# Kernel tuning notes

Hardware: AMD Instinct MI355X
Metric: run time of the kernel (lower is better)

The kernel has to match this reference:

```python
import jax, jax.numpy as jnp
import numpy as np

EMBED = 50
SEQ = 100
NLABEL = 15
HID = 20
VOCAB = 50000
BATCH = 8192


def gru_scan(xs, W, U, b, return_sequences):
    """Keras GRUCell (reset_after=True, gate order z,r,h).
    xs: (B, T, D). W: (D, 3H), U: (H, 3H), b: (2, 3H) [input bias, recurrent bias].
    """
    B = xs.shape[0]
    H = U.shape[0]
    bi, br = b[0], b[1]
    h0 = jnp.zeros((B, H), dtype=xs.dtype)

    def step(h, x_t):
        mx = x_t @ W + bi                      # (B, 3H)
        mh = h @ U + br                        # (B, 3H)
        xz, xr, xh = mx[:, :H], mx[:, H:2*H], mx[:, 2*H:]
        hz, hr, hh_ = mh[:, :H], mh[:, H:2*H], mh[:, 2*H:]
        z = jax.nn.sigmoid(xz + hz)
        r = jax.nn.sigmoid(xr + hr)
        hh = jnp.tanh(xh + r * hh_)
        h_new = z * h + (1.0 - z) * hh
        return h_new, h_new

    xs_t = jnp.swapaxes(xs, 0, 1)              # (T, B, D)
    h_last, hs = jax.lax.scan(step, h0, xs_t)
    if return_sequences:
        return jnp.swapaxes(hs, 0, 1)          # (B, T, H)
    return h_last                               # (B, H)


def setup_inputs() -> dict:
    key = jax.random.key(0)
    ks = jax.random.split(key, 9)
    s = 0.05
    return {
        "x": jax.random.randint(ks[0], (BATCH, SEQ), 0, VOCAB),
        "emb_table": jax.random.normal(ks[1], (VOCAB, EMBED), jnp.float32) * s,
        "W1": jax.random.normal(ks[2], (EMBED, 3 * HID), jnp.float32) * s,
        "U1": jax.random.normal(ks[3], (HID, 3 * HID), jnp.float32) * s,
        "b1": jnp.zeros((2, 3 * HID), jnp.float32),
        "W2": jax.random.normal(ks[4], (HID, 3 * HID), jnp.float32) * s,
        "U2": jax.random.normal(ks[5], (HID, 3 * HID), jnp.float32) * s,
        "b2": jnp.zeros((2, 3 * HID), jnp.float32),
        "Wd": jax.random.normal(ks[6], (HID, NLABEL), jnp.float32) * s,
        "bd": jnp.zeros((NLABEL,), jnp.float32),
        "drop_rate": 0,
    }


def reference(x, emb_table, W1, U1, b1, W2, U2, b2, Wd, bd, drop_rate):
    emb = emb_table[x]                               # (B, T, E)
    seq = gru_scan(emb, W1, U1, b1, return_sequences=True)   # (B, T, H)
    enc = gru_scan(seq, W2, U2, b2, return_sequences=False)  # (B, H)
    # drop_rate == 0 -> tf.nn.dropout is identity
    logits = enc @ Wd + bd                           # (B, 15)
    return logits
```

## Files before the change

### kernel.cpp

```cpp
#include <hip/hip_runtime.h>
#include <hip/hip_bf16.h>
#include <hip/hip_fp16.h>

#define SEQ_T 100
#define HID 20
#define EMB_D 50
#define VOCAB_N 50000
#define TABW 60
#define NTILE 3125
#define BBLK 782

typedef short sh8 __attribute__((ext_vector_type(8)));
typedef float f4  __attribute__((ext_vector_type(4)));

#define OFF_U1P 0
#define OFF_W2P 600
#define OFF_U2P 1200
#define OFF_B1  3600
#define OFF_B2  3720
#define OFF_WD  3840
#define OFF_BD  4140
#define OFF_TAB 4160

__device__ __forceinline__ float ldf(const void* p, int i, int isf) {
  return isf ? ((const float*)p)[i]
             : __bfloat162float(((const __hip_bfloat16*)p)[i]);
}
__device__ __forceinline__ short f2bf(float f) {
  unsigned u = __float_as_uint(f);
  u += 0x7fffu + ((u >> 16) & 1u);
  return (short)(u >> 16);
}
__device__ __forceinline__ float rdl(float v, int l) {
  return __uint_as_float(__builtin_amdgcn_readlane(__float_as_uint(v), l));
}
__device__ __forceinline__ int detect_isf(const void* emb) {
  uint4 dv = ((const uint4*)emb)[threadIdx.x & 63];
  int big = 0;
#pragma unroll
  for (int i = 0; i < 4; ++i) {
    unsigned w = ((const unsigned*)&dv)[i];
    big |= (((w >> 7) & 0xFF) >= 140) | (((w >> 23) & 0xFF) >= 140);
  }
  return (__ballot(big) != 0ull) ? 1 : 0;
}

__global__ __launch_bounds__(256) void build_table(
    const void* __restrict__ emb, const void* __restrict__ W1,
    const void* __restrict__ b1,
    const void* __restrict__ U1, const void* __restrict__ W2,
    const void* __restrict__ U2, const void* __restrict__ b2,
    const void* __restrict__ Wd, const void* __restrict__ bd,
    float* __restrict__ ws)
{
  const int isf = detect_isf(emb);
  if (blockIdx.x == 0) {
    const int t = threadIdx.x;
    unsigned* wsu = (unsigned*)ws;
    for (int i = t; i < 600; i += 256) {
      const int j = i / 10, p = i % 10;
      const int k0 = 2 * p, k1 = 2 * p + 1;
#define PK(M) ((unsigned)__half_as_ushort(__float2half_rn(ldf(M, k0 * 60 + j, isf))) | \
               ((unsigned)__half_as_ushort(__float2half_rn(ldf(M, k1 * 60 + j, isf))) << 16))
      wsu[OFF_U1P + i] = PK(U1);
      wsu[OFF_W2P + i] = PK(W2);
      wsu[OFF_U2P + i] = PK(U2);
#undef PK
    }
    for (int i = t; i < 120; i += 256) {
      ws[OFF_B1 + i] = ldf(b1, i, isf);
      ws[OFF_B2 + i] = ldf(b2, i, isf);
    }
    for (int i = t; i < 300; i += 256) ws[OFF_WD + i] = ldf(Wd, i, isf);
    for (int i = t; i < 15;  i += 256) ws[OFF_BD + i] = ldf(bd, i, isf);
  }

  const int L = threadIdx.x & 63, q = L >> 4, c = L & 15;
  const int wid = blockIdx.x * 4 + (threadIdx.x >> 6);
  float* __restrict__ tab = ws + OFF_TAB;

  __shared__ int4 sB[64][8];
  if (threadIdx.x < 64) {
#pragma unroll
    for (int nt = 0; nt < 4; ++nt) {
      const int col = nt * 16 + c;
      sh8 B0, B1;
#pragma unroll
      for (int jj = 0; jj < 8; ++jj) {
        const int k0 = q * 8 + jj, k1 = 32 + q * 8 + jj;
        B0[jj] = (col < TABW) ? f2bf(ldf(W1, k0 * TABW + col, isf)) : (short)0;
        B1[jj] = (col < TABW && k1 < EMB_D)
                     ? f2bf(ldf(W1, k1 * TABW + col, isf)) : (short)0;
      }
      sB[L][nt * 2]     = *(const int4*)&B0;
      sB[L][nt * 2 + 1] = *(const int4*)&B1;
    }
  }
  float bi[4];
#pragma unroll
  for (int nt = 0; nt < 4; ++nt) {
    const int col = nt * 16 + c;
    bi[nt] = (col < TABW) ? ldf(b1, col, isf) : 0.f;
  }
  __syncthreads();

  for (int tile = wid; tile < NTILE; tile += BBLK * 4) {
    const int v0 = tile * 16;
    sh8 A0, A1;
#pragma unroll
    for (int jj = 0; jj < 8; ++jj) { A0[jj] = 0; A1[jj] = 0; }
    if (!isf) {
      const unsigned short* eb = (const unsigned short*)emb;
      const size_t rb = (size_t)(v0 + c) * EMB_D;
#pragma unroll
      for (int i = 0; i < 4; ++i) {
        unsigned d = *(const unsigned*)(eb + rb + q * 8 + 2 * i);
        A0[2 * i] = (short)(d & 0xffff); A0[2 * i + 1] = (short)(d >> 16);
      }
      const int k1b = 32 + q * 8;
#pragma unroll
      for (int i = 0; i < 4; ++i) {
        const int k = k1b + 2 * i;
        if (k + 1 < EMB_D) {
          unsigned d = *(const unsigned*)(eb + rb + k);
          A1[2 * i] = (short)(d & 0xffff); A1[2 * i + 1] = (short)(d >> 16);
        }
      }
    } else {
      const float* ef = (const float*)emb;
      const size_t rb = (size_t)(v0 + c) * EMB_D;
#pragma unroll
      for (int jj = 0; jj < 8; ++jj) {
        const int k0 = q * 8 + jj, k1 = 32 + q * 8 + jj;
        A0[jj] = f2bf(ef[rb + k0]);
        A1[jj] = (k1 < EMB_D) ? f2bf(ef[rb + k1]) : (short)0;
      }
    }
#pragma unroll
    for (int nt = 0; nt < 4; ++nt) {
      int4 b0i = sB[L][nt * 2], b1i = sB[L][nt * 2 + 1];
      sh8 B0 = *(const sh8*)&b0i, B1 = *(const sh8*)&b1i;
      const int col = nt * 16 + c;
      f4 acc = { bi[nt], bi[nt], bi[nt], bi[nt] };
      acc = __builtin_amdgcn_mfma_f32_16x16x32_bf16(A0, B0, acc, 0, 0, 0);
      acc = __builtin_amdgcn_mfma_f32_16x16x32_bf16(A1, B1, acc, 0, 0, 0);
      if (col < TABW) {
#pragma unroll
        for (int r = 0; r < 4; ++r)
          tab[(size_t)(v0 + q * 4 + r) * TABW + col] = acc[r];
      }
    }
  }
}

__global__ __launch_bounds__(256, 8) void gru_main(
    const int* __restrict__ x, const float* __restrict__ ws,
    const void* __restrict__ emb, void* __restrict__ out)
{
  const int isf = detect_isf(emb);
  const int j = threadIdx.x & 63;
  const int e = __builtin_amdgcn_readfirstlane(blockIdx.x * 4 + (threadIdx.x >> 6));
  const int jc = j < TABW ? j : 0;

  const int* xr = x + (size_t)e * SEQ_T;
  const float* tab = ws + OFF_TAB;
  const int o1 = jc * 40;
  const int jc4 = jc * 4;
  const int a1 = ((j - 20) & 63) * 4;
  const int a2 = ((j + 40) & 63) * 4;
  const float br1 = ws[OFF_B1 + 60 + jc];
  const float bi2 = ws[OFF_B2 + jc];
  const float br2 = ws[OFF_B2 + 60 + jc];
  float h2out;

  asm volatile(
    "global_load_dwordx4 v[10:13], %[o1], %[wsp] offset:0\n\t"
    "global_load_dwordx4 v[14:17], %[o1], %[wsp] offset:16\n\t"
    "global_load_dwordx2 v[18:19], %[o1], %[wsp] offset:32\n\t"
    "v_add_u32 v44, 0x960, %[o1]\n\t"
    "v_add_u32 v45, 0x12c0, %[o1]\n\t"
    "global_load_dwordx4 v[20:23], v44, %[wsp] offset:0\n\t"
    "global_load_dwordx4 v[24:27], v44, %[wsp] offset:16\n\t"
    "global_load_dwordx2 v[28:29], v44, %[wsp] offset:32\n\t"
    "global_load_dwordx4 v[30:33], v45, %[wsp] offset:0\n\t"
    "global_load_dwordx4 v[34:37], v45, %[wsp] offset:16\n\t"
    "global_load_dwordx2 v[38:39], v45, %[wsp] offset:32\n\t"
    "s_mov_b64 s[20:21], 0\n\ts_mov_b64 s[22:23], 0\n\t"
    "s_mov_b64 s[24:25], 0\n\ts_mov_b64 s[26:27], 0\n\t"
    "s_mov_b64 s[28:29], 0\n\t"
    "s_mov_b64 s[30:31], 0\n\ts_mov_b64 s[32:33], 0\n\t"
    "s_mov_b64 s[34:35], 0\n\ts_mov_b64 s[36:37], 0\n\t"
    "s_mov_b64 s[38:39], 0\n\t"
    "v_mov_b32 v40, 0\n\t"
    "v_mov_b32 v41, 0\n\t"
    "s_load_dword s65, %[xp], 0x0\n\t"
    "s_load_dword s66, %[xp], 0x4\n\t"
    "s_waitcnt lgkmcnt(0)\n\t"
    "s_mul_i32 s65, s65, 240\n\t"
    "s_mul_i32 s66, s66, 240\n\t"
    "v_add_u32 v50, s65, %[jc4]\n\t"
    "global_load_dword v42, v50, %[tabp]\n\t"
    "v_add_u32 v50, s66, %[jc4]\n\t"
    "global_load_dword v43, v50, %[tabp]\n\t"
    "s_load_dword s65, %[xp], 0x8\n\t"
    "s_movk_i32 s64, 0xc\n\t"
    "s_movk_i32 s67, 0x64\n\t"
    "s_waitcnt vmcnt(0)\n\t"
    "0:\n\t"
    "v_mov_b32 v44, %[br1]\n\t"
    "v_dot2_f32_f16 v44, s20, v10, v44\n\t"
    "v_dot2_f32_f16 v44, s21, v11, v44\n\t"
    "v_dot2_f32_f16 v44, s22, v12, v44\n\t"
    "v_dot2_f32_f16 v44, s23, v13, v44\n\t"
    "v_dot2_f32_f16 v44, s24, v14, v44\n\t"
    "v_dot2_f32_f16 v44, s25, v15, v44\n\t"
    "v_dot2_f32_f16 v44, s26, v16, v44\n\t"
    "v_dot2_f32_f16 v44, s27, v17, v44\n\t"
    "v_dot2_f32_f16 v44, s28, v18, v44\n\t"
    "v_dot2_f32_f16 v44, s29, v19, v44\n\t"
    "v_add_f32 v45, v42, v44\n\t"
    "v_mul_f32 v45, 0xbfb8aa3b, v45\n\t"
    "v_exp_f32 v45, v45\n\t"
    "s_nop 1\n\t"
    "v_add_f32 v45, 1.0, v45\n\t"
    "v_rcp_f32 v45, v45\n\t"
    "s_nop 1\n\t"
    "ds_bpermute_b32 v46, %[a1], v45\n\t"
    "s_waitcnt lgkmcnt(0)\n\t"
    "v_fma_f32 v47, v46, v44, v42\n\t"
    "v_mul_f32 v47, 0x4038aa3b, v47\n\t"
    "v_exp_f32 v47, v47\n\t"
    "s_nop 1\n\t"
    "v_add_f32 v47, 1.0, v47\n\t"
    "v_rcp_f32 v47, v47\n\t"
    "s_nop 1\n\t"
    "v_fma_f32 v47, -2.0, v47, 1.0\n\t"
    "ds_bpermute_b32 v46, %[a2], v47\n\t"
    "s_waitcnt lgkmcnt(0)\n\t"
    "v_sub_f32 v48, v40, v46\n\t"
    "v_fma_f32 v40, v45, v48, v46\n\t"
    "s_nop 1\n\t"
    "v_cvt_f16_f32 v46, v40\n\t"
    "s_nop 1\n\t"
    "ds_swizzle_b32 v47, v46 offset:0x041F\n\t"
    "s_waitcnt lgkmcnt(0)\n\t"
    "v_pack_b32_f16 v46, v46, v47\n\t"
    "s_nop 1\n\t"
    "v_readlane_b32 s20, v46, 0\n\t"
    "v_readlane_b32 s21, v46, 2\n\t"
    "v_readlane_b32 s22, v46, 4\n\t"
    "v_readlane_b32 s23, v46, 6\n\t"
    "v_readlane_b32 s24, v46, 8\n\t"
    "v_readlane_b32 s25, v46, 10\n\t"
    "v_readlane_b32 s26, v46, 12\n\t"
    "v_readlane_b32 s27, v46, 14\n\t"
    "v_readlane_b32 s28, v46, 16\n\t"
    "v_readlane_b32 s29, v46, 18\n\t"
    "s_mul_i32 s66, s65, 240\n\t"
    "v_add_u32 v50, s66, %[jc4]\n\t"
    "s_waitcnt vmcnt(0)\n\t"
    "v_mov_b32 v42, v43\n\t"
    "global_load_dword v43, v50, %[tabp]\n\t"
    "s_min_u32 s64, s64, 396\n\t"
    "s_load_dword s65, %[xp], s64\n\t"
    "s_add_u32 s64, s64, 4\n\t"
    "v_mov_b32 v44, %[bi2]\n\t"
    "v_mov_b32 v48, %[br2]\n\t"
    "v_dot2_f32_f16 v44, s20, v20, v44\n\t"
    "v_dot2_f32_f16 v48, s30, v30, v48\n\t"
    "v_dot2_f32_f16 v44, s21, v21, v44\n\t"
    "v_dot2_f32_f16 v48, s31, v31, v48\n\t"
    "v_dot2_f32_f16 v44, s22, v22, v44\n\t"
    "v_dot2_f32_f16 v48, s32, v32, v48\n\t"
    "v_dot2_f32_f16 v44, s23, v23, v44\n\t"
    "v_dot2_f32_f16 v48, s33, v33, v48\n\t"
    "v_dot2_f32_f16 v44, s24, v24, v44\n\t"
    "v_dot2_f32_f16 v48, s34, v34, v48\n\t"
    "v_dot2_f32_f16 v44, s25, v25, v44\n\t"
    "v_dot2_f32_f16 v48, s35, v35, v48\n\t"
    "v_dot2_f32_f16 v44, s26, v26, v44\n\t"
    "v_dot2_f32_f16 v48, s36, v36, v48\n\t"
    "v_dot2_f32_f16 v44, s27, v27, v44\n\t"
    "v_dot2_f32_f16 v48, s37, v37, v48\n\t"
    "v_dot2_f32_f16 v44, s28, v28, v44\n\t"
    "v_dot2_f32_f16 v48, s38, v38, v48\n\t"
    "v_dot2_f32_f16 v44, s29, v29, v44\n\t"
    "v_dot2_f32_f16 v48, s39, v39, v48\n\t"
    "v_add_f32 v45, v44, v48\n\t"
    "v_mul_f32 v45, 0xbfb8aa3b, v45\n\t"
    "v_exp_f32 v45, v45\n\t"
    "s_nop 1\n\t"
    "v_add_f32 v45, 1.0, v45\n\t"
    "v_rcp_f32 v45, v45\n\t"
    "s_nop 1\n\t"
    "ds_bpermute_b32 v46, %[a1], v45\n\t"
    "s_waitcnt lgkmcnt(0)\n\t"
    "v_fma_f32 v47, v46, v48, v44\n\t"
    "v_mul_f32 v47, 0x4038aa3b, v47\n\t"
    "v_exp_f32 v47, v47\n\t"
    "s_nop 1\n\t"
    "v_add_f32 v47, 1.0, v47\n\t"
    "v_rcp_f32 v47, v47\n\t"
    "s_nop 1\n\t"
    "v_fma_f32 v47, -2.0, v47, 1.0\n\t"
    "ds_bpermute_b32 v46, %[a2], v47\n\t"
    "s_waitcnt lgkmcnt(0)\n\t"
    "v_sub_f32 v49, v41, v46\n\t"
    "v_fma_f32 v41, v45, v49, v46\n\t"
    "s_nop 1\n\t"
    "v_cvt_f16_f32 v46, v41\n\t"
    "s_nop 1\n\t"
    "ds_swizzle_b32 v47, v46 offset:0x041F\n\t"
    "s_waitcnt lgkmcnt(0)\n\t"
    "v_pack_b32_f16 v46, v46, v47\n\t"
    "s_nop 1\n\t"
    "v_readlane_b32 s30, v46, 0\n\t"
    "v_readlane_b32 s31, v46, 2\n\t"
    "v_readlane_b32 s32, v46, 4\n\t"
    "v_readlane_b32 s33, v46, 6\n\t"
    "v_readlane_b32 s34, v46, 8\n\t"
    "v_readlane_b32 s35, v46, 10\n\t"
    "v_readlane_b32 s36, v46, 12\n\t"
    "v_readlane_b32 s37, v46, 14\n\t"
    "v_readlane_b32 s38, v46, 16\n\t"
    "v_readlane_b32 s39, v46, 18\n\t"
    "s_sub_u32 s67, s67, 1\n\t"
    "s_cmp_lg_u32 s67, 0\n\t"
    "s_cbranch_scc1 0b\n\t"
    "s_waitcnt vmcnt(0) lgkmcnt(0)\n\t"
    "v_mov_b32 %[h2o], v41\n\t"
    : [h2o] "=v"(h2out)
    : [wsp] "s"(ws), [xp] "s"(xr), [tabp] "s"(tab),
      [o1] "v"(o1), [jc4] "v"(jc4), [a1] "v"(a1), [a2] "v"(a2),
      [br1] "v"(br1), [bi2] "v"(bi2), [br2] "v"(br2)
    : "memory", "vcc", "scc",
      "v10","v11","v12","v13","v14","v15","v16","v17","v18","v19",
      "v20","v21","v22","v23","v24","v25","v26","v27","v28","v29",
      "v30","v31","v32","v33","v34","v35","v36","v37","v38","v39",
      "v40","v41","v42","v43","v44","v45","v46","v47","v48","v49","v50",
      "s20","s21","s22","s23","s24","s25","s26","s27","s28","s29",
      "s30","s31","s32","s33","s34","s35","s36","s37","s38","s39",
      "s64","s65","s66","s67");

  if (j < 15) {
    float a = ws[OFF_BD + j];
#pragma unroll
    for (int k = 0; k < HID; ++k)
      a = fmaf(rdl(h2out, k), ws[OFF_WD + k * 15 + j], a);
    if (isf) ((float*)out)[(size_t)e * 15 + j] = a;
    else ((__hip_bfloat16*)out)[(size_t)e * 15 + j] = __float2bfloat16(a);
  }
}

extern "C" void kernel_launch(void* const* d_in, const int* in_sizes, int n_in,
                              void* d_out, int out_size, void* d_ws, size_t ws_size,
                              hipStream_t stream) {
  const int* x    = (const int*)d_in[0];
  const void* emb = d_in[1];
  const void* W1  = d_in[2];
  const void* U1  = d_in[3];
  const void* b1  = d_in[4];
  const void* W2  = d_in[5];
  const void* U2  = d_in[6];
  const void* b2  = d_in[7];
  const void* Wd  = d_in[8];
  const void* bd  = d_in[9];
  float* ws = (float*)d_ws;

  build_table<<<BBLK, 256, 0, stream>>>(
      emb, W1, b1, U1, W2, U2, b2, Wd, bd, ws);
  gru_main<<<2048, 256, 0, stream>>>(x, ws, emb, d_out);
}
```

Before: 240.6 us.

## Rewrite GRU recurrence as batched MFMA per wave over 8 sequences

Replaces the per-sequence dot2/readlane scalar recurrence with a wave that processes 8 sequences at once. Each step runs the input projection, recurrent matmuls and both GRU layers through 16x16x32 MFMA instructions, passing hidden state through LDS. The precomputed projected-embedding table is dropped in favour of a padded bf16 copy of the embeddings, so W1 is applied on the fly each step. This raises compute per step and leaves half of each MFMA tile idle, in exchange for far fewer waves and removal of the serial scalar dot-product chain.

```diff
diff --git a/kernel.cpp b/kernel.cpp
--- a/kernel.cpp
+++ b/kernel.cpp
@@ -3,36 +3,26 @@
 #include <hip/hip_fp16.h>
 
 #define SEQ_T 100
-#define HID 20
-#define EMB_D 50
 #define VOCAB_N 50000
-#define TABW 60
-#define NTILE 3125
-#define BBLK 782
-
-typedef short sh8 __attribute__((ext_vector_type(8)));
-typedef float f4  __attribute__((ext_vector_type(4)));
-
-#define OFF_U1P 0
-#define OFF_W2P 600
-#define OFF_U2P 1200
-#define OFF_B1  3600
-#define OFF_B2  3720
-#define OFF_WD  3840
-#define OFF_BD  4140
-#define OFF_TAB 4160
+
+typedef short    sh8 __attribute__((ext_vector_type(8)));
+typedef _Float16 hf8 __attribute__((ext_vector_type(8)));
+typedef float    f4  __attribute__((ext_vector_type(4)));
+
+#define OFF_BF   0
+#define OFF_BIAS 7680
+#define OFF_WD   7936
+#define OFF_BD   8236
+#define OFF_TABA 8256
 
 __device__ __forceinline__ float ldf(const void* p, int i, int isf) {
   return isf ? ((const float*)p)[i]
              : __bfloat162float(((const __hip_bfloat16*)p)[i]);
 }
-__device__ __forceinline__ short f2bf(float f) {
+__device__ __forceinline__ unsigned short f2bf(float f) {
   unsigned u = __float_as_uint(f);
   u += 0x7fffu + ((u >> 16) & 1u);
-  return (short)(u >> 16);
-}
-__device__ __forceinline__ float rdl(float v, int l) {
-  return __uint_as_float(__builtin_amdgcn_readlane(__float_as_uint(v), l));
+  return (unsigned short)(u >> 16);
 }
 __device__ __forceinline__ int detect_isf(const void* emb) {
   uint4 dv = ((const uint4*)emb)[threadIdx.x & 63];
@@ -44,8 +34,18 @@
   }
   return (__ballot(big) != 0ull) ? 1 : 0;
 }
-
-__global__ __launch_bounds__(256) void build_table(
+__device__ __forceinline__ float vexp2(float x) {
+  float r; asm("v_exp_f32 %0, %1\n\ts_nop 1" : "=v"(r) : "v"(x)); return r;
+}
+__device__ __forceinline__ float vrcp(float x) {
+  float r; asm("v_rcp_f32 %0, %1\n\ts_nop 1" : "=v"(r) : "v"(x)); return r;
+}
+__device__ __forceinline__ unsigned short cvw(const void* M, int idx, int isf, int fp16) {
+  float f = ldf(M, idx, isf);
+  return fp16 ? __half_as_ushort(__float2half_rn(f)) : f2bf(f);
+}
+
+__global__ __launch_bounds__(256) void build_pre(
     const void* __restrict__ emb, const void* __restrict__ W1,
     const void* __restrict__ b1,
     const void* __restrict__ U1, const void* __restrict__ W2,
@@ -54,301 +54,206 @@
     float* __restrict__ ws)
 {
   const int isf = detect_isf(emb);
+  unsigned* wsu = (unsigned*)ws;
   if (blockIdx.x == 0) {
-    const int t = threadIdx.x;
-    unsigned* wsu = (unsigned*)ws;
-    for (int i = t; i < 600; i += 256) {
-      const int j = i / 10, p = i % 10;
-      const int k0 = 2 * p, k1 = 2 * p + 1;
-#define PK(M) ((unsigned)__half_as_ushort(__float2half_rn(ldf(M, k0 * 60 + j, isf))) | \
-               ((unsigned)__half_as_ushort(__float2half_rn(ldf(M, k1 * 60 + j, isf))) << 16))
-      wsu[OFF_U1P + i] = PK(U1);
-      wsu[OFF_W2P + i] = PK(W2);
-      wsu[OFF_U2P + i] = PK(U2);
-#undef PK
-    }
-    for (int i = t; i < 120; i += 256) {
-      ws[OFF_B1 + i] = ldf(b1, i, isf);
-      ws[OFF_B2 + i] = ldf(b2, i, isf);
-    }
-    for (int i = t; i < 300; i += 256) ws[OFF_WD + i] = ldf(Wd, i, isf);
-    for (int i = t; i < 15;  i += 256) ws[OFF_BD + i] = ldf(bd, i, isf);
-  }
-
-  const int L = threadIdx.x & 63, q = L >> 4, c = L & 15;
-  const int wid = blockIdx.x * 4 + (threadIdx.x >> 6);
-  float* __restrict__ tab = ws + OFF_TAB;
-
-  __shared__ int4 sB[64][8];
-  if (threadIdx.x < 64) {
-#pragma unroll
-    for (int nt = 0; nt < 4; ++nt) {
-      const int col = nt * 16 + c;
-      sh8 B0, B1;
-#pragma unroll
-      for (int jj = 0; jj < 8; ++jj) {
-        const int k0 = q * 8 + jj, k1 = 32 + q * 8 + jj;
-        B0[jj] = (col < TABW) ? f2bf(ldf(W1, k0 * TABW + col, isf)) : (short)0;
-        B1[jj] = (col < TABW && k1 < EMB_D)
-                     ? f2bf(ldf(W1, k1 * TABW + col, isf)) : (short)0;
+    for (int i = threadIdx.x; i < 7680; i += 256) {
+      const int f = i >> 8, L = (i >> 2) & 63, dw = i & 3;
+      const void* M; int kt, nt, kmax, fp16;
+      if (f < 6)       { M = W1; kt = 0; nt = f;      kmax = 50; fp16 = 0; }
+      else if (f < 12) { M = W1; kt = 1; nt = f - 6;  kmax = 50; fp16 = 0; }
+      else if (f < 18) { M = U1; kt = 0; nt = f - 12; kmax = 20; fp16 = 1; }
+      else if (f < 24) { M = W2; kt = 0; nt = f - 18; kmax = 20; fp16 = 1; }
+      else             { M = U2; kt = 0; nt = f - 24; kmax = 20; fp16 = 1; }
+      const int n = nt * 16 + (L & 15);
+      const int gc = n < 32 ? n : (n < 64 ? n - 12 : n - 24);
+      const int gcv = (n & 31) < 20;
+      const int k0 = kt * 32 + ((L >> 4) * 8) + dw * 2;
+      unsigned lo = 0, hi = 0;
+      if (gcv && k0 < kmax)     lo = cvw(M, k0 * 60 + gc, isf, fp16);
+      if (gcv && k0 + 1 < kmax) hi = cvw(M, (k0 + 1) * 60 + gc, isf, fp16);
+      wsu[OFF_BF + i] = lo | (hi << 16);
+    }
+    {
+      int i = threadIdx.x;
+      const int half = i >> 7;
+      const void* B = half ? b2 : b1;
+      const int n = i & 127;
+      float v = 0.f;
+      if (n < 64)      { int gc = n < 32 ? n : n - 12;
+                         if ((n & 31) < 20) v = ldf(B, gc, isf) + ldf(B, 60 + gc, isf); }
+      else if (n < 96) { int cc = n - 64; if (cc < 20) v = ldf(B, 40 + cc, isf); }
+      else             { int cc = n - 96; if (cc < 20) v = ldf(B, 100 + cc, isf); }
+      ws[OFF_BIAS + i] = v;
+    }
+    for (int i = threadIdx.x; i < 300; i += 256) ws[OFF_WD + i] = ldf(Wd, i, isf);
+    for (int i = threadIdx.x; i < 15;  i += 256) ws[OFF_BD + i] = ldf(bd, i, isf);
+  }
+  const int total = VOCAB_N * 32;
+  for (int d = blockIdx.x * 256 + threadIdx.x; d < total; d += 256 * 256) {
+    const int row = d >> 5, c2 = d & 31;
+    unsigned v = 0;
+    if (c2 < 25) {
+      if (!isf) v = ((const unsigned*)emb)[row * 25 + c2];
+      else {
+        const float* ef = (const float*)emb;
+        v = (unsigned)f2bf(ef[row * 50 + 2 * c2]) |
+            ((unsigned)f2bf(ef[row * 50 + 2 * c2 + 1]) << 16);
       }
-      sB[L][nt * 2]     = *(const int4*)&B0;
-      sB[L][nt * 2 + 1] = *(const int4*)&B1;
-    }
-  }
-  float bi[4];
-#pragma unroll
-  for (int nt = 0; nt < 4; ++nt) {
-    const int col = nt * 16 + c;
-    bi[nt] = (col < TABW) ? ldf(b1, col, isf) : 0.f;
-  }
-  __syncthreads();
-
-  for (int tile = wid; tile < NTILE; tile += BBLK * 4) {
-    const int v0 = tile * 16;
-    sh8 A0, A1;
-#pragma unroll
-    for (int jj = 0; jj < 8; ++jj) { A0[jj] = 0; A1[jj] = 0; }
-    if (!isf) {
-      const unsigned short* eb = (const unsigned short*)emb;
-      const size_t rb = (size_t)(v0 + c) * EMB_D;
-#pragma unroll
-      for (int i = 0; i < 4; ++i) {
-        unsigned d = *(const unsigned*)(eb + rb + q * 8 + 2 * i);
-        A0[2 * i] = (short)(d & 0xffff); A0[2 * i + 1] = (short)(d >> 16);
-      }
-      const int k1b = 32 + q * 8;
-#pragma unroll
-      for (int i = 0; i < 4; ++i) {
-        const int k = k1b + 2 * i;
-        if (k + 1 < EMB_D) {
-          unsigned d = *(const unsigned*)(eb + rb + k);
-          A1[2 * i] = (short)(d & 0xffff); A1[2 * i + 1] = (short)(d >> 16);
-        }
-      }
-    } else {
-      const float* ef = (const float*)emb;
-      const size_t rb = (size_t)(v0 + c) * EMB_D;
-#pragma unroll
-      for (int jj = 0; jj < 8; ++jj) {
-        const int k0 = q * 8 + jj, k1 = 32 + q * 8 + jj;
-        A0[jj] = f2bf(ef[rb + k0]);
-        A1[jj] = (k1 < EMB_D) ? f2bf(ef[rb + k1]) : (short)0;
-      }
-    }
-#pragma unroll
-    for (int nt = 0; nt < 4; ++nt) {
-      int4 b0i = sB[L][nt * 2], b1i = sB[L][nt * 2 + 1];
-      sh8 B0 = *(const sh8*)&b0i, B1 = *(const sh8*)&b1i;
-      const int col = nt * 16 + c;
-      f4 acc = { bi[nt], bi[nt], bi[nt], bi[nt] };
-      acc = __builtin_amdgcn_mfma_f32_16x16x32_bf16(A0, B0, acc, 0, 0, 0);
-      acc = __builtin_amdgcn_mfma_f32_16x16x32_bf16(A1, B1, acc, 0, 0, 0);
-      if (col < TABW) {
-#pragma unroll
-        for (int r = 0; r < 4; ++r)
-          tab[(size_t)(v0 + q * 4 + r) * TABW + col] = acc[r];
-      }
-    }
-  }
-}
-
-__global__ __launch_bounds__(256, 8) void gru_main(
+    }
+    wsu[OFF_TABA + d] = v;
+  }
+}
+
+__global__ __launch_bounds__(64) void gru_main(
     const int* __restrict__ x, const float* __restrict__ ws,
     const void* __restrict__ emb, void* __restrict__ out)
 {
   const int isf = detect_isf(emb);
-  const int j = threadIdx.x & 63;
-  const int e = __builtin_amdgcn_readfirstlane(blockIdx.x * 4 + (threadIdx.x >> 6));
-  const int jc = j < TABW ? j : 0;
-
-  const int* xr = x + (size_t)e * SEQ_T;
-  const float* tab = ws + OFF_TAB;
-  const int o1 = jc * 40;
-  const int jc4 = jc * 4;
-  const int a1 = ((j - 20) & 63) * 4;
-  const int a2 = ((j + 40) & 63) * 4;
-  const float br1 = ws[OFF_B1 + 60 + jc];
-  const float bi2 = ws[OFF_B2 + jc];
-  const float br2 = ws[OFF_B2 + 60 + jc];
-  float h2out;
-
-  asm volatile(
-    "global_load_dwordx4 v[10:13], %[o1], %[wsp] offset:0\n\t"
-    "global_load_dwordx4 v[14:17], %[o1], %[wsp] offset:16\n\t"
-    "global_load_dwordx2 v[18:19], %[o1], %[wsp] offset:32\n\t"
-    "v_add_u32 v44, 0x960, %[o1]\n\t"
-    "v_add_u32 v45, 0x12c0, %[o1]\n\t"
-    "global_load_dwordx4 v[20:23], v44, %[wsp] offset:0\n\t"
-    "global_load_dwordx4 v[24:27], v44, %[wsp] offset:16\n\t"
-    "global_load_dwordx2 v[28:29], v44, %[wsp] offset:32\n\t"
-    "global_load_dwordx4 v[30:33], v45, %[wsp] offset:0\n\t"
-    "global_load_dwordx4 v[34:37], v45, %[wsp] offset:16\n\t"
-    "global_load_dwordx2 v[38:39], v45, %[wsp] offset:32\n\t"
-    "s_mov_b64 s[20:21], 0\n\ts_mov_b64 s[22:23], 0\n\t"
-    "s_mov_b64 s[24:25], 0\n\ts_mov_b64 s[26:27], 0\n\t"
-    "s_mov_b64 s[28:29], 0\n\t"
-    "s_mov_b64 s[30:31], 0\n\ts_mov_b64 s[32:33], 0\n\t"
-    "s_mov_b64 s[34:35], 0\n\ts_mov_b64 s[36:37], 0\n\t"
-    "s_mov_b64 s[38:39], 0\n\t"
-    "v_mov_b32 v40, 0\n\t"
-    "v_mov_b32 v41, 0\n\t"
-    "s_load_dword s65, %[xp], 0x0\n\t"
-    "s_load_dword s66, %[xp], 0x4\n\t"
-    "s_waitcnt lgkmcnt(0)\n\t"
-    "s_mul_i32 s65, s65, 240\n\t"
-    "s_mul_i32 s66, s66, 240\n\t"
-    "v_add_u32 v50, s65, %[jc4]\n\t"
-    "global_load_dword v42, v50, %[tabp]\n\t"
-    "v_add_u32 v50, s66, %[jc4]\n\t"
-    "global_load_dword v43, v50, %[tabp]\n\t"
-    "s_load_dword s65, %[xp], 0x8\n\t"
-    "s_movk_i32 s64, 0xc\n\t"
-    "s_movk_i32 s67, 0x64\n\t"
-    "s_waitcnt vmcnt(0)\n\t"
-    "0:\n\t"
-    "v_mov_b32 v44, %[br1]\n\t"
-    "v_dot2_f32_f16 v44, s20, v10, v44\n\t"
-    "v_dot2_f32_f16 v44, s21, v11, v44\n\t"
-    "v_dot2_f32_f16 v44, s22, v12, v44\n\t"
-    "v_dot2_f32_f16 v44, s23, v13, v44\n\t"
-    "v_dot2_f32_f16 v44, s24, v14, v44\n\t"
-    "v_dot2_f32_f16 v44, s25, v15, v44\n\t"
-    "v_dot2_f32_f16 v44, s26, v16, v44\n\t"
-    "v_dot2_f32_f16 v44, s27, v17, v44\n\t"
-    "v_dot2_f32_f16 v44, s28, v18, v44\n\t"
-    "v_dot2_f32_f16 v44, s29, v19, v44\n\t"
-    "v_add_f32 v45, v42, v44\n\t"
-    "v_mul_f32 v45, 0xbfb8aa3b, v45\n\t"
-    "v_exp_f32 v45, v45\n\t"
-    "s_nop 1\n\t"
-    "v_add_f32 v45, 1.0, v45\n\t"
-    "v_rcp_f32 v45, v45\n\t"
-    "s_nop 1\n\t"
-    "ds_bpermute_b32 v46, %[a1], v45\n\t"
-    "s_waitcnt lgkmcnt(0)\n\t"
-    "v_fma_f32 v47, v46, v44, v42\n\t"
-    "v_mul_f32 v47, 0x4038aa3b, v47\n\t"
-    "v_exp_f32 v47, v47\n\t"
-    "s_nop 1\n\t"
-    "v_add_f32 v47, 1.0, v47\n\t"
-    "v_rcp_f32 v47, v47\n\t"
-    "s_nop 1\n\t"
-    "v_fma_f32 v47, -2.0, v47, 1.0\n\t"
-    "ds_bpermute_b32 v46, %[a2], v47\n\t"
-    "s_waitcnt lgkmcnt(0)\n\t"
-    "v_sub_f32 v48, v40, v46\n\t"
-    "v_fma_f32 v40, v45, v48, v46\n\t"
-    "s_nop 1\n\t"
-    "v_cvt_f16_f32 v46, v40\n\t"
-    "s_nop 1\n\t"
-    "ds_swizzle_b32 v47, v46 offset:0x041F\n\t"
-    "s_waitcnt lgkmcnt(0)\n\t"
-    "v_pack_b32_f16 v46, v46, v47\n\t"
-    "s_nop 1\n\t"
-    "v_readlane_b32 s20, v46, 0\n\t"
-    "v_readlane_b32 s21, v46, 2\n\t"
-    "v_readlane_b32 s22, v46, 4\n\t"
-    "v_readlane_b32 s23, v46, 6\n\t"
-    "v_readlane_b32 s24, v46, 8\n\t"
-    "v_readlane_b32 s25, v46, 10\n\t"
-    "v_readlane_b32 s26, v46, 12\n\t"
-    "v_readlane_b32 s27, v46, 14\n\t"
-    "v_readlane_b32 s28, v46, 16\n\t"
-    "v_readlane_b32 s29, v46, 18\n\t"
-    "s_mul_i32 s66, s65, 240\n\t"
-    "v_add_u32 v50, s66, %[jc4]\n\t"
-    "s_waitcnt vmcnt(0)\n\t"
-    "v_mov_b32 v42, v43\n\t"
-    "global_load_dword v43, v50, %[tabp]\n\t"
-    "s_min_u32 s64, s64, 396\n\t"
-    "s_load_dword s65, %[xp], s64\n\t"
-    "s_add_u32 s64, s64, 4\n\t"
-    "v_mov_b32 v44, %[bi2]\n\t"
-    "v_mov_b32 v48, %[br2]\n\t"
-    "v_dot2_f32_f16 v44, s20, v20, v44\n\t"
-    "v_dot2_f32_f16 v48, s30, v30, v48\n\t"
-    "v_dot2_f32_f16 v44, s21, v21, v44\n\t"
-    "v_dot2_f32_f16 v48, s31, v31, v48\n\t"
-    "v_dot2_f32_f16 v44, s22, v22, v44\n\t"
-    "v_dot2_f32_f16 v48, s32, v32, v48\n\t"
-    "v_dot2_f32_f16 v44, s23, v23, v44\n\t"
-    "v_dot2_f32_f16 v48, s33, v33, v48\n\t"
-    "v_dot2_f32_f16 v44, s24, v24, v44\n\t"
-    "v_dot2_f32_f16 v48, s34, v34, v48\n\t"
-    "v_dot2_f32_f16 v44, s25, v25, v44\n\t"
-    "v_dot2_f32_f16 v48, s35, v35, v48\n\t"
-    "v_dot2_f32_f16 v44, s26, v26, v44\n\t"
-    "v_dot2_f32_f16 v48, s36, v36, v48\n\t"
-    "v_dot2_f32_f16 v44, s27, v27, v44\n\t"
-    "v_dot2_f32_f16 v48, s37, v37, v48\n\t"
-    "v_dot2_f32_f16 v44, s28, v28, v44\n\t"
-    "v_dot2_f32_f16 v48, s38, v38, v48\n\t"
-    "v_dot2_f32_f16 v44, s29, v29, v44\n\t"
-    "v_dot2_f32_f16 v48, s39, v39, v48\n\t"
-    "v_add_f32 v45, v44, v48\n\t"
-    "v_mul_f32 v45, 0xbfb8aa3b, v45\n\t"
-    "v_exp_f32 v45, v45\n\t"
-    "s_nop 1\n\t"
-    "v_add_f32 v45, 1.0, v45\n\t"
-    "v_rcp_f32 v45, v45\n\t"
-    "s_nop 1\n\t"
-    "ds_bpermute_b32 v46, %[a1], v45\n\t"
-    "s_waitcnt lgkmcnt(0)\n\t"
-    "v_fma_f32 v47, v46, v48, v44\n\t"
-    "v_mul_f32 v47, 0x4038aa3b, v47\n\t"
-    "v_exp_f32 v47, v47\n\t"
-    "s_nop 1\n\t"
-    "v_add_f32 v47, 1.0, v47\n\t"
-    "v_rcp_f32 v47, v47\n\t"
-    "s_nop 1\n\t"
-    "v_fma_f32 v47, -2.0, v47, 1.0\n\t"
-    "ds_bpermute_b32 v46, %[a2], v47\n\t"
-    "s_waitcnt lgkmcnt(0)\n\t"
-    "v_sub_f32 v49, v41, v46\n\t"
-    "v_fma_f32 v41, v45, v49, v46\n\t"
-    "s_nop 1\n\t"
-    "v_cvt_f16_f32 v46, v41\n\t"
-    "s_nop 1\n\t"
-    "ds_swizzle_b32 v47, v46 offset:0x041F\n\t"
-    "s_waitcnt lgkmcnt(0)\n\t"
-    "v_pack_b32_f16 v46, v46, v47\n\t"
-    "s_nop 1\n\t"
-    "v_readlane_b32 s30, v46, 0\n\t"
-    "v_readlane_b32 s31, v46, 2\n\t"
-    "v_readlane_b32 s32, v46, 4\n\t"
-    "v_readlane_b32 s33, v46, 6\n\t"
-    "v_readlane_b32 s34, v46, 8\n\t"
-    "v_readlane_b32 s35, v46, 10\n\t"
-    "v_readlane_b32 s36, v46, 12\n\t"
-    "v_readlane_b32 s37, v46, 14\n\t"
-    "v_readlane_b32 s38, v46, 16\n\t"
-    "v_readlane_b32 s39, v46, 18\n\t"
-    "s_sub_u32 s67, s67, 1\n\t"
-    "s_cmp_lg_u32 s67, 0\n\t"
-    "s_cbranch_scc1 0b\n\t"
-    "s_waitcnt vmcnt(0) lgkmcnt(0)\n\t"
-    "v_mov_b32 %[h2o], v41\n\t"
-    : [h2o] "=v"(h2out)
-    : [wsp] "s"(ws), [xp] "s"(xr), [tabp] "s"(tab),
-      [o1] "v"(o1), [jc4] "v"(jc4), [a1] "v"(a1), [a2] "v"(a2),
-      [br1] "v"(br1), [bi2] "v"(bi2), [br2] "v"(br2)
-    : "memory", "vcc", "scc",
-      "v10","v11","v12","v13","v14","v15","v16","v17","v18","v19",
-      "v20","v21","v22","v23","v24","v25","v26","v27","v28","v29",
-      "v30","v31","v32","v33","v34","v35","v36","v37","v38","v39",
-      "v40","v41","v42","v43","v44","v45","v46","v47","v48","v49","v50",
-      "s20","s21","s22","s23","s24","s25","s26","s27","s28","s29",
-      "s30","s31","s32","s33","s34","s35","s36","s37","s38","s39",
-      "s64","s65","s66","s67");
-
-  if (j < 15) {
-    float a = ws[OFF_BD + j];
-#pragma unroll
-    for (int k = 0; k < HID; ++k)
-      a = fmaf(rdl(h2out, k), ws[OFF_WD + k * 15 + j], a);
-    if (isf) ((float*)out)[(size_t)e * 15 + j] = a;
-    else ((__hip_bfloat16*)out)[(size_t)e * 15 + j] = __float2bfloat16(a);
+  const int l = threadIdx.x, c = l & 15, q = l >> 4;
+  const int wid = blockIdx.x;
+
+  __shared__ _Float16 hb1[16][40];
+  __shared__ _Float16 hb2[16][40];
+  __shared__ float    fb[16][21];
+  for (int i = l; i < 640; i += 64) {
+    ((_Float16*)hb1)[i] = (_Float16)0.f;
+    ((_Float16*)hb2)[i] = (_Float16)0.f;
+  }
+  asm volatile("s_waitcnt lgkmcnt(0)" ::: "memory");
+
+  const uint4* wsu4 = (const uint4*)ws;
+  sh8 w1f[12]; hf8 u1f[6], w2f[6], u2f[6];
+#pragma unroll
+  for (int f = 0; f < 12; ++f) { uint4 u = wsu4[f * 64 + l];        w1f[f] = *(sh8*)&u; }
+#pragma unroll
+  for (int f = 0; f < 6; ++f)  { uint4 u = wsu4[(12 + f) * 64 + l]; u1f[f] = *(hf8*)&u; }
+#pragma unroll
+  for (int f = 0; f < 6; ++f)  { uint4 u = wsu4[(18 + f) * 64 + l]; w2f[f] = *(hf8*)&u; }
+#pragma unroll
+  for (int f = 0; f < 6; ++f)  { uint4 u = wsu4[(24 + f) * 64 + l]; u2f[f] = *(hf8*)&u; }
+
+  float bzr1[4], bzr2[4], bxh1[2], brh1[2], bxh2[2], brh2[2];
+#pragma unroll
+  for (int nt = 0; nt < 4; ++nt) {
+    bzr1[nt] = ws[OFF_BIAS + nt * 16 + c];
+    bzr2[nt] = ws[OFF_BIAS + 128 + nt * 16 + c];
+  }
+#pragma unroll
+  for (int i = 0; i < 2; ++i) {
+    bxh1[i] = ws[OFF_BIAS + 64 + i * 16 + c];
+    brh1[i] = ws[OFF_BIAS + 96 + i * 16 + c];
+    bxh2[i] = ws[OFF_BIAS + 192 + i * 16 + c];
+    brh2[i] = ws[OFF_BIAS + 224 + i * 16 + c];
+  }
+
+  const uint4* ta = (const uint4*)(ws + OFF_TABA);
+  const int* xb = x + (size_t)(wid * 8 + (c & 7)) * SEQ_T;
+  int xn = xb[0];
+  int x2 = xb[1];
+  uint4 ea0 = ta[xn * 8 + q], ea1 = ta[xn * 8 + 4 + q];
+  xn = x2; x2 = xb[2];
+
+  f4 h1t[2] = {{0.f,0.f,0.f,0.f},{0.f,0.f,0.f,0.f}};
+  f4 h2t[2] = {{0.f,0.f,0.f,0.f},{0.f,0.f,0.f,0.f}};
+  hf8 h1a = {(_Float16)0.f};
+  hf8 h2a = {(_Float16)0.f};
+
+  for (int t = 0; t < SEQ_T; ++t) {
+    uint4 na0 = ta[xn * 8 + q], na1 = ta[xn * 8 + 4 + q];
+    const int tpp = (t + 3 < SEQ_T) ? t + 3 : SEQ_T - 1;
+    const int xnn = xb[tpp];
+    const sh8 eA = *(const sh8*)&ea0, eB = *(const sh8*)&ea1;
+
+    f4 azr[4], axh[2], arh[2];
+#pragma unroll
+    for (int nt = 0; nt < 4; ++nt) {
+      f4 a = { bzr1[nt], bzr1[nt], bzr1[nt], bzr1[nt] };
+      a = __builtin_amdgcn_mfma_f32_16x16x32_bf16(eA, w1f[nt], a, 0, 0, 0);
+      a = __builtin_amdgcn_mfma_f32_16x16x32_bf16(eB, w1f[6 + nt], a, 0, 0, 0);
+      a = __builtin_amdgcn_mfma_f32_16x16x32_f16(h1a, u1f[nt], a, 0, 0, 0);
+      azr[nt] = a;
+    }
+#pragma unroll
+    for (int i = 0; i < 2; ++i) {
+      f4 a = { bxh1[i], bxh1[i], bxh1[i], bxh1[i] };
+      a = __builtin_amdgcn_mfma_f32_16x16x32_bf16(eA, w1f[4 + i], a, 0, 0, 0);
+      a = __builtin_amdgcn_mfma_f32_16x16x32_bf16(eB, w1f[10 + i], a, 0, 0, 0);
+      axh[i] = a;
+      f4 b = { brh1[i], brh1[i], brh1[i], brh1[i] };
+      b = __builtin_amdgcn_mfma_f32_16x16x32_f16(h1a, u1f[4 + i], b, 0, 0, 0);
+      arh[i] = b;
+    }
+#pragma unroll
+    for (int i = 0; i < 2; ++i)
+#pragma unroll
+      for (int r = 0; r < 4; ++r) {
+        float z  = vrcp(1.f + vexp2(azr[i][r] * -1.44269504f));
+        float rg = vrcp(1.f + vexp2(azr[2 + i][r] * -1.44269504f));
+        float hp = fmaf(rg, arh[i][r], axh[i][r]);
+        float hc = fmaf(-2.f, vrcp(1.f + vexp2(hp * 2.88539008f)), 1.f);
+        float hn = fmaf(z, h1t[i][r] - hc, hc);
+        h1t[i][r] = hn;
+        if (c + 16 * i < 20) hb1[q * 4 + r][c + 16 * i] = (_Float16)hn;
+      }
+    asm volatile("s_waitcnt lgkmcnt(0)" ::: "memory");
+    h1a = *(const hf8*)&hb1[c][q * 8];
+
+#pragma unroll
+    for (int nt = 0; nt < 4; ++nt) {
+      f4 a = { bzr2[nt], bzr2[nt], bzr2[nt], bzr2[nt] };
+      a = __builtin_amdgcn_mfma_f32_16x16x32_f16(h1a, w2f[nt], a, 0, 0, 0);
+      a = __builtin_amdgcn_mfma_f32_16x16x32_f16(h2a, u2f[nt], a, 0, 0, 0);
+      azr[nt] = a;
+    }
+#pragma unroll
+    for (int i = 0; i < 2; ++i) {
+      f4 a = { bxh2[i], bxh2[i], bxh2[i], bxh2[i] };
+      a = __builtin_amdgcn_mfma_f32_16x16x32_f16(h1a, w2f[4 + i], a, 0, 0, 0);
+      axh[i] = a;
+      f4 b = { brh2[i], brh2[i], brh2[i], brh2[i] };
+      b = __builtin_amdgcn_mfma_f32_16x16x32_f16(h2a, u2f[4 + i], b, 0, 0, 0);
+      arh[i] = b;
+    }
+#pragma unroll
+    for (int i = 0; i < 2; ++i)
+#pragma unroll
+      for (int r = 0; r < 4; ++r) {
+        float z  = vrcp(1.f + vexp2(azr[i][r] * -1.44269504f));
+        float rg = vrcp(1.f + vexp2(azr[2 + i][r] * -1.44269504f));
+        float hp = fmaf(rg, arh[i][r], axh[i][r]);
+        float hc = fmaf(-2.f, vrcp(1.f + vexp2(hp * 2.88539008f)), 1.f);
+        float hn = fmaf(z, h2t[i][r] - hc, hc);
+        h2t[i][r] = hn;
+        if (c + 16 * i < 20) hb2[q * 4 + r][c + 16 * i] = (_Float16)hn;
+      }
+    asm volatile("s_waitcnt lgkmcnt(0)" ::: "memory");
+    h2a = *(const hf8*)&hb2[c][q * 8];
+
+    ea0 = na0; ea1 = na1; xn = x2; x2 = xnn;
+  }
+
+#pragma unroll
+  for (int i = 0; i < 2; ++i)
+#pragma unroll
+    for (int r = 0; r < 4; ++r)
+      if (q < 2 && c + 16 * i < 20) fb[q * 4 + r][c + 16 * i] = h2t[i][r];
+  asm volatile("s_waitcnt lgkmcnt(0)" ::: "memory");
+  const int e2 = l >> 3, j0 = (l & 7) * 2;
+  float a0 = ws[OFF_BD + j0];
+  float a1 = (j0 + 1 < 15) ? ws[OFF_BD + j0 + 1] : 0.f;
+#pragma unroll
+  for (int k = 0; k < 20; ++k) {
+    float h = fb[e2][k];
+    a0 = fmaf(h, ws[OFF_WD + k * 15 + j0], a0);
+    if (j0 + 1 < 15) a1 = fmaf(h, ws[OFF_WD + k * 15 + j0 + 1], a1);
+  }
+  const size_t ob = (size_t)(wid * 8 + e2) * 15;
+  if (isf) {
+    ((float*)out)[ob + j0] = a0;
+    if (j0 + 1 < 15) ((float*)out)[ob + j0 + 1] = a1;
+  } else {
+    ((__hip_bfloat16*)out)[ob + j0] = __float2bfloat16(a0);
+    if (j0 + 1 < 15) ((__hip_bfloat16*)out)[ob + j0 + 1] = __float2bfloat16(a1);
   }
 }
 
@@ -367,7 +272,6 @@
   const void* bd  = d_in[9];
   float* ws = (float*)d_ws;
 
-  build_table<<<BBLK, 256, 0, stream>>>(
-      emb, W1, b1, U1, W2, U2, b2, Wd, bd, ws);
-  gru_main<<<2048, 256, 0, stream>>>(x, ws, emb, d_out);
-}
+  build_pre<<<256, 256, 0, stream>>>(emb, W1, b1, U1, W2, U2, b2, Wd, bd, ws);
+  gru_main<<<1024, 64, 0, stream>>>(x, ws, emb, d_out);
+}
```

Measured after the change: 272.0 us. +13.0%, slower.
